# Kernel optimization log

Hardware: AMD Instinct MI355X
Metric: run time of the kernel (lower is better)

Reference implementation:

```python
import jax, jax.numpy as jnp
import numpy as np

N_NODES = 20000
N_EDGES = 640000
N_FEATS = 3703
HIDDEN = 50
N_CLASSES = 6
N_KENN_LAYERS = 3
# clause: not C_c(x) OR C_c(y) OR not Cite(x,y)  -> literal signs
SIGNS = np.array([-1.0, 1.0, -1.0], dtype=np.float32)


def setup_inputs() -> dict:
    key = jax.random.key(0)
    ks = jax.random.split(key, 12)
    features = jax.random.normal(ks[0], (N_NODES, N_FEATS), dtype=jnp.float32)
    relations = jax.random.normal(ks[1], (N_EDGES, 1), dtype=jnp.float32)
    sx = jax.random.randint(ks[2], (N_EDGES,), 0, N_NODES)
    sy = jax.random.randint(ks[3], (N_EDGES,), 0, N_NODES)

    def dense(k, fan_in, fan_out):
        return jax.random.normal(k, (fan_in, fan_out), dtype=jnp.float32) / np.sqrt(fan_in).astype(np.float32)

    W1 = dense(ks[4], N_FEATS, HIDDEN); b1 = jnp.zeros((HIDDEN,), jnp.float32)
    W2 = dense(ks[5], HIDDEN, HIDDEN);  b2 = jnp.zeros((HIDDEN,), jnp.float32)
    W3 = dense(ks[6], HIDDEN, HIDDEN);  b3 = jnp.zeros((HIDDEN,), jnp.float32)
    W4 = dense(ks[7], HIDDEN, N_CLASSES); b4 = jnp.zeros((N_CLASSES,), jnp.float32)
    # one learnable clause weight per class-clause, per KENN layer (init 0.5 as in KENN)
    clause_weights = jnp.full((N_KENN_LAYERS, N_CLASSES), 0.5, dtype=jnp.float32)
    return dict(features=features, relations=relations, sx=sx, sy=sy,
                W1=W1, b1=b1, W2=W2, b2=b2, W3=W3, b3=b3, W4=W4, b4=b4,
                clause_weights=clause_weights)


def _kenn_layer(z, relations, sx, sy, cw):
    # z: [N, C]; relations: [E, 1]; cw: [C] clause weights
    n = z.shape[0]
    zx = z[sx]                                   # [E, C] gather head literals
    zy = z[sy]                                   # [E, C] gather tail literals
    rel = jnp.broadcast_to(relations, (relations.shape[0], z.shape[1]))  # [E, C]
    signs = jnp.asarray(SIGNS)
    # signed literal preactivations per clause: [E, C, 3]
    v = jnp.stack([-zx, zy, -rel], axis=-1)
    # KENN boost: delta = w_c * softmax(signed preacts) * sign
    d = cw[None, :, None] * jax.nn.softmax(v, axis=-1) * signs[None, None, :]
    # scatter unary deltas back to nodes (relation delta is discarded)
    dz = jax.ops.segment_sum(d[..., 0], sx, num_segments=n)
    dz = dz + jax.ops.segment_sum(d[..., 1], sy, num_segments=n)
    return z + dz


def reference(features, relations, sx, sy, W1, b1, W2, b2, W3, b3, W4, b4, clause_weights):
    # MLP preactivations (dropout inactive at inference)
    x = jax.nn.relu(features @ W1 + b1)
    x = jax.nn.relu(x @ W2 + b2)
    x = jax.nn.relu(x @ W3 + b3)
    z = x @ W4 + b4                               # [N, 6]
    for i in range(N_KENN_LAYERS):
        z = _kenn_layer(z, relations, sx, sy, clause_weights[i])
    return jax.nn.softmax(z, axis=-1)
```

## Files before the change

kernel.cpp:

```cpp
#include <hip/hip_runtime.h>

#define M_NODES 20000
#define K_FEATS 3703
#define PADK 3712
#define NH 50
#define NC 6
#define N_EDGES_C 640000
#define NKB 116

typedef __attribute__((ext_vector_type(8))) __bf16 bf16x8;
typedef __attribute__((ext_vector_type(4))) float f32x4;

__global__ void k_packB(const float* __restrict__ W1, unsigned short* __restrict__ Bh,
                        unsigned short* __restrict__ Bl) {
  int idx = blockIdx.x * 256 + threadIdx.x;
  if (idx >= NKB * 4 * 64 * 8) return;
  int j = idx & 7;
  int lane = (idx >> 3) & 63;
  int t = (idx >> 9) & 3;
  int kb = idx >> 11;
  int k = kb * 32 + (lane >> 4) * 8 + j;
  int c = t * 16 + (lane & 15);
  float v = (k < K_FEATS && c < NH) ? W1[k * NH + c] : 0.f;
  __bf16 hb = (__bf16)v;
  float hf = (float)hb;
  __bf16 lb = (__bf16)(v - hf);
  Bh[idx] = *(unsigned short*)&hb;
  Bl[idx] = *(unsigned short*)&lb;
}

__global__ __launch_bounds__(256) void k_gemm1(const float* __restrict__ A,
    const unsigned short* __restrict__ Bph, const unsigned short* __restrict__ Bpl,
    float* __restrict__ part, int KS) {
  const int lane = threadIdx.x & 63;
  const int w = threadIdx.x >> 6;
  const int row0 = blockIdx.x * 128 + w * 32;
  const int s = blockIdx.y;
  const int ks = s * KS;
  const int ke = (ks + KS < PADK) ? ks + KS : PADK;
  const int nsteps = (ke - ks) >> 5;
  const int g = lane >> 4;
  const int rl = lane & 15;
  const int r0c = min(row0 + rl, M_NODES - 1);
  const int r1c = min(row0 + 16 + rl, M_NODES - 1);
  const float* a0p = A + (size_t)r0c * K_FEATS + 8 * g;
  const float* a1p = A + (size_t)r1c * K_FEATS + 8 * g;
  const bf16x8* BH = (const bf16x8*)Bph;
  const bf16x8* BL = (const bf16x8*)Bpl;

  f32x4 acc[2][4];
  #pragma unroll
  for (int i = 0; i < 2; ++i)
    #pragma unroll
    for (int t = 0; t < 4; ++t) acc[i][t] = (f32x4){0.f, 0.f, 0.f, 0.f};

  #define LOADA(d0, d1, k0) {                                     \
    d0[0] = *(const float4*)(a0p + (k0));                         \
    d0[1] = *(const float4*)(a0p + (k0) + 4);                     \
    d1[0] = *(const float4*)(a1p + (k0));                         \
    d1[1] = *(const float4*)(a1p + (k0) + 4); }
  #define LOADAG(d0, d1, k0) {                                    \
    _Pragma("unroll") for (int j = 0; j < 8; ++j) {               \
      int gk = (k0) + 8 * g + j;                                  \
      float v0 = (gk < K_FEATS) ? a0p[(k0) + j] : 0.f;            \
      float v1 = (gk < K_FEATS) ? a1p[(k0) + j] : 0.f;            \
      ((float*)d0)[j] = v0; ((float*)d1)[j] = v1; } }
  #define LDSEL(d0, d1, k0) {                                     \
    if ((k0) + 32 > K_FEATS) { LOADAG(d0, d1, k0) }               \
    else { LOADA(d0, d1, k0) } }

  #define BODY(sa0, sa1, k0) {                                    \
    const int kb4 = ((k0) >> 5) * 4;                              \
    bf16x8 bh0 = BH[(kb4 + 0) * 64 + lane];                       \
    bf16x8 bh1 = BH[(kb4 + 1) * 64 + lane];                       \
    bf16x8 bh2 = BH[(kb4 + 2) * 64 + lane];                       \
    bf16x8 bh3 = BH[(kb4 + 3) * 64 + lane];                       \
    bf16x8 bl0 = BL[(kb4 + 0) * 64 + lane];                       \
    bf16x8 bl1 = BL[(kb4 + 1) * 64 + lane];                       \
    bf16x8 bl2 = BL[(kb4 + 2) * 64 + lane];                       \
    bf16x8 bl3 = BL[(kb4 + 3) * 64 + lane];                       \
    bf16x8 ah0, al0, ah1, al1;                                    \
    _Pragma("unroll") for (int j = 0; j < 8; ++j) {               \
      float xv = ((const float*)sa0)[j];                          \
      __bf16 hb = (__bf16)xv; float hf = (float)hb;               \
      ah0[j] = hb; al0[j] = (__bf16)(xv - hf);                    \
      float yv = ((const float*)sa1)[j];                          \
      __bf16 hb2 = (__bf16)yv; float hf2 = (float)hb2;            \
      ah1[j] = hb2; al1[j] = (__bf16)(yv - hf2);                  \
    }                                                             \
    acc[0][0] = __builtin_amdgcn_mfma_f32_16x16x32_bf16(ah0, bh0, acc[0][0], 0, 0, 0); \
    acc[0][1] = __builtin_amdgcn_mfma_f32_16x16x32_bf16(ah0, bh1, acc[0][1], 0, 0, 0); \
    acc[0][2] = __builtin_amdgcn_mfma_f32_16x16x32_bf16(ah0, bh2, acc[0][2], 0, 0, 0); \
    acc[0][3] = __builtin_amdgcn_mfma_f32_16x16x32_bf16(ah0, bh3, acc[0][3], 0, 0, 0); \
    acc[1][0] = __builtin_amdgcn_mfma_f32_16x16x32_bf16(ah1, bh0, acc[1][0], 0, 0, 0); \
    acc[1][1] = __builtin_amdgcn_mfma_f32_16x16x32_bf16(ah1, bh1, acc[1][1], 0, 0, 0); \
    acc[1][2] = __builtin_amdgcn_mfma_f32_16x16x32_bf16(ah1, bh2, acc[1][2], 0, 0, 0); \
    acc[1][3] = __builtin_amdgcn_mfma_f32_16x16x32_bf16(ah1, bh3, acc[1][3], 0, 0, 0); \
    acc[0][0] = __builtin_amdgcn_mfma_f32_16x16x32_bf16(al0, bh0, acc[0][0], 0, 0, 0); \
    acc[0][1] = __builtin_amdgcn_mfma_f32_16x16x32_bf16(al0, bh1, acc[0][1], 0, 0, 0); \
    acc[0][2] = __builtin_amdgcn_mfma_f32_16x16x32_bf16(al0, bh2, acc[0][2], 0, 0, 0); \
    acc[0][3] = __builtin_amdgcn_mfma_f32_16x16x32_bf16(al0, bh3, acc[0][3], 0, 0, 0); \
    acc[1][0] = __builtin_amdgcn_mfma_f32_16x16x32_bf16(al1, bh0, acc[1][0], 0, 0, 0); \
    acc[1][1] = __builtin_amdgcn_mfma_f32_16x16x32_bf16(al1, bh1, acc[1][1], 0, 0, 0); \
    acc[1][2] = __builtin_amdgcn_mfma_f32_16x16x32_bf16(al1, bh2, acc[1][2], 0, 0, 0); \
    acc[1][3] = __builtin_amdgcn_mfma_f32_16x16x32_bf16(al1, bh3, acc[1][3], 0, 0, 0); \
    acc[0][0] = __builtin_amdgcn_mfma_f32_16x16x32_bf16(ah0, bl0, acc[0][0], 0, 0, 0); \
    acc[0][1] = __builtin_amdgcn_mfma_f32_16x16x32_bf16(ah0, bl1, acc[0][1], 0, 0, 0); \
    acc[0][2] = __builtin_amdgcn_mfma_f32_16x16x32_bf16(ah0, bl2, acc[0][2], 0, 0, 0); \
    acc[0][3] = __builtin_amdgcn_mfma_f32_16x16x32_bf16(ah0, bl3, acc[0][3], 0, 0, 0); \
    acc[1][0] = __builtin_amdgcn_mfma_f32_16x16x32_bf16(ah1, bl0, acc[1][0], 0, 0, 0); \
    acc[1][1] = __builtin_amdgcn_mfma_f32_16x16x32_bf16(ah1, bl1, acc[1][1], 0, 0, 0); \
    acc[1][2] = __builtin_amdgcn_mfma_f32_16x16x32_bf16(ah1, bl2, acc[1][2], 0, 0, 0); \
    acc[1][3] = __builtin_amdgcn_mfma_f32_16x16x32_bf16(ah1, bl3, acc[1][3], 0, 0, 0); }

  float4 p0a[2], p0b[2], p1a[2], p1b[2], p2a[2], p2b[2];
  LDSEL(p0a, p0b, ks);
  if (nsteps > 1) LDSEL(p1a, p1b, ks + 32);
  if (nsteps > 2) LDSEL(p2a, p2b, ks + 64);

  int t = 0;
  for (; t + 3 <= nsteps; t += 3) {
    const int k0 = ks + (t << 5);
    BODY(p0a, p0b, k0);
    if (t + 3 < nsteps) LDSEL(p0a, p0b, k0 + 96);
    BODY(p1a, p1b, k0 + 32);
    if (t + 4 < nsteps) LDSEL(p1a, p1b, k0 + 128);
    BODY(p2a, p2b, k0 + 64);
    if (t + 5 < nsteps) LDSEL(p2a, p2b, k0 + 160);
  }
  if (t < nsteps)     BODY(p0a, p0b, ks + (t << 5));
  if (t + 1 < nsteps) BODY(p1a, p1b, ks + ((t + 1) << 5));
  #undef LOADA
  #undef LOADAG
  #undef LDSEL
  #undef BODY

  float* p = part + (size_t)s * 1000000;
  #pragma unroll
  for (int i = 0; i < 2; ++i) {
    #pragma unroll
    for (int t2 = 0; t2 < 4; ++t2) {
      int col = t2 * 16 + rl;
      if (col < NH) {
        int rowb = row0 + i * 16 + g * 4;
        f32x4 v = acc[i][t2];
        #pragma unroll
        for (int q = 0; q < 4; ++q) {
          int row = rowb + q;
          if (row < M_NODES) p[row * NH + col] = v[q];
        }
      }
    }
  }
}

__global__ void k_epi(const float* __restrict__ part, const float* __restrict__ b1,
                      float* __restrict__ x1, int S) {
  int i = blockIdx.x * 256 + threadIdx.x;
  if (i >= M_NODES * NH) return;
  float v = b1[i % NH];
  for (int s = 0; s < S; ++s) v += part[(size_t)s * 1000000 + i];
  x1[i] = fmaxf(v, 0.f);
}

__global__ __launch_bounds__(256) void k_mlp(const float* __restrict__ x1,
    const float* __restrict__ W2, const float* __restrict__ b2,
    const float* __restrict__ W3, const float* __restrict__ b3,
    const float* __restrict__ W4, const float* __restrict__ b4,
    float* __restrict__ z) {
  __shared__ float lX[32 * 51];
  __shared__ float lW2[50 * 52];
  __shared__ float lW3[50 * 52];
  __shared__ float lW4[50 * 8];
  const int tid = threadIdx.x;
  const int row0 = blockIdx.x * 32;
  for (int idx = tid; idx < 2500; idx += 256) {
    int k = idx / 50, n = idx % 50;
    lW2[k * 52 + n] = W2[idx];
    lW3[k * 52 + n] = W3[idx];
  }
  for (int idx = tid; idx < 300; idx += 256) {
    int k = idx / 6, n = idx % 6;
    lW4[k * 8 + n] = W4[idx];
  }
  for (int idx = tid; idx < 1600; idx += 256) {
    int r = idx / 50, k = idx % 50;
    int gr = row0 + r;
    lX[r * 51 + k] = (gr < M_NODES) ? x1[gr * 50 + k] : 0.f;
  }
  __syncthreads();
  const int r = tid >> 3, cg = tid & 7;
  float x[50];
  #pragma unroll
  for (int k = 0; k < 50; ++k) x[k] = lX[r * 51 + k];

  for (int layer = 0; layer < 2; ++layer) {
    const float* lW = (layer == 0) ? lW2 : lW3;
    const float* bg = (layer == 0) ? b2 : b3;
    float acc[7];
    #pragma unroll
    for (int j = 0; j < 7; ++j) {
      int n = cg + 8 * j;
      acc[j] = (n < 50) ? bg[n] : 0.f;
    }
    #pragma unroll
    for (int k = 0; k < 50; ++k) {
      float xk = x[k];
      #pragma unroll
      for (int j = 0; j < 7; ++j) {
        int n = cg + 8 * j;
        if (n < 50) acc[j] = fmaf(xk, lW[k * 52 + n], acc[j]);
      }
    }
    __syncthreads();
    #pragma unroll
    for (int j = 0; j < 7; ++j) {
      int n = cg + 8 * j;
      if (n < 50) lX[r * 51 + n] = fmaxf(acc[j], 0.f);
    }
    __syncthreads();
    #pragma unroll
    for (int k = 0; k < 50; ++k) x[k] = lX[r * 51 + k];
  }
  if (cg < 6) {
    float accz = b4[cg];
    #pragma unroll
    for (int k = 0; k < 50; ++k) accz = fmaf(x[k], lW4[k * 8 + cg], accz);
    int gr = row0 + r;
    if (gr < M_NODES) z[gr * 6 + cg] = accz;
  }
}

__global__ void k_count(const int* __restrict__ sx, const int* __restrict__ sy,
                        int* __restrict__ cnt) {
  int e = blockIdx.x * 256 + threadIdx.x;
  if (e >= N_EDGES_C) return;
  atomicAdd(&cnt[sx[e]], 1);
  atomicAdd(&cnt[sy[e]], 1);
}

__global__ __launch_bounds__(1024) void k_scan(const int* __restrict__ cnt,
                                               int* __restrict__ off,
                                               int* __restrict__ cur) {
  __shared__ int sums[1024];
  int t = threadIdx.x;
  int base = t * 20;
  int local[20];
  int s = 0;
  #pragma unroll
  for (int j = 0; j < 20; ++j) {
    int idx = base + j;
    int v = (idx < M_NODES) ? cnt[idx] : 0;
    local[j] = s;
    s += v;
  }
  sums[t] = s;
  __syncthreads();
  for (int d = 1; d < 1024; d <<= 1) {
    int v = (t >= d) ? sums[t - d] : 0;
    __syncthreads();
    sums[t] += v;
    __syncthreads();
  }
  int excl = sums[t] - s;
  #pragma unroll
  for (int j = 0; j < 20; ++j) {
    int idx = base + j;
    if (idx < M_NODES) {
      int o = excl + local[j];
      off[idx] = o;
      cur[idx] = o;
    }
  }
  if (t == 1023) off[M_NODES] = sums[1023];
}

__global__ void k_scatter(const int* __restrict__ sx, const int* __restrict__ sy,
                          const float* __restrict__ rel,
                          int* __restrict__ cur, int2* __restrict__ ent) {
  int e = blockIdx.x * 256 + threadIdx.x;
  if (e >= N_EDGES_C) return;
  int a = sx[e], b = sy[e];
  int rb = __float_as_int(rel[e]);
  int p = atomicAdd(&cur[a], 1);
  ent[p] = make_int2((b << 1), rb);
  int q = atomicAdd(&cur[b], 1);
  ent[q] = make_int2((a << 1) | 1, rb);
}

__global__ __launch_bounds__(256) void k_gather(const float* __restrict__ z,
    const int* __restrict__ off, const int2* __restrict__ ent,
    const float* __restrict__ cw, float* __restrict__ partial) {
  int t = blockIdx.x * 256 + threadIdx.x;
  if (t >= M_NODES * 8) return;
  int s = t & 7;
  int n = t >> 3;
  int o0 = off[n];
  int deg = off[n + 1] - o0;
  int lo = o0 + ((deg * s) >> 3);
  int hi = o0 + ((deg * (s + 1)) >> 3);

  const float2* zr = (const float2*)(z + n * 6);
  float2 a0 = zr[0], a1 = zr[1], a2 = zr[2];
  float znv[6] = {a0.x, a0.y, a1.x, a1.y, a2.x, a2.y};
  float w[6];
  #pragma unroll
  for (int c = 0; c < 6; ++c) w[c] = cw[c];
  float dz[6] = {0.f, 0.f, 0.f, 0.f, 0.f, 0.f};

  for (int i = lo; i < hi; ++i) {
    int2 e2 = ent[i];
    int partner = e2.x >> 1;
    int side = e2.x & 1;
    float r = __int_as_float(e2.y);
    const float2* zp2 = (const float2*)(z + partner * 6);
    float2 p0 = zp2[0], p1 = zp2[1], p2 = zp2[2];
    float zpv[6] = {p0.x, p0.y, p1.x, p1.y, p2.x, p2.y};
    float v2 = -r;
    #pragma unroll
    for (int c = 0; c < 6; ++c) {
      float zx = side ? zpv[c] : znv[c];
      float zy = side ? znv[c] : zpv[c];
      float v0 = -zx, v1 = zy;
      float m = fmaxf(fmaxf(v0, v1), v2);
      float e0 = __expf(v0 - m);
      float e1 = __expf(v1 - m);
      float e2v = __expf(v2 - m);
      float inv = w[c] / (e0 + e1 + e2v);
      dz[c] += (side ? e1 : -e0) * inv;
    }
  }
  float* pp = partial + (size_t)s * 120000 + n * 6;
  #pragma unroll
  for (int c = 0; c < 6; ++c) pp[c] = dz[c];
}

__global__ void k_combine(const float* __restrict__ zc, const float* __restrict__ partial,
                          float* __restrict__ zn) {
  int i = blockIdx.x * 256 + threadIdx.x;
  if (i >= M_NODES * NC) return;
  float v = zc[i];
  #pragma unroll
  for (int s = 0; s < 8; ++s) v += partial[(size_t)s * 120000 + i];
  zn[i] = v;
}

__global__ void k_combine_softmax(const float* __restrict__ zc,
                                  const float* __restrict__ partial,
                                  float* __restrict__ out) {
  int n = blockIdx.x * 256 + threadIdx.x;
  if (n >= M_NODES) return;
  float v[6];
  #pragma unroll
  for (int c = 0; c < 6; ++c) v[c] = zc[n * 6 + c];
  #pragma unroll
  for (int s = 0; s < 8; ++s) {
    const float* pp = partial + (size_t)s * 120000 + n * 6;
    #pragma unroll
    for (int c = 0; c < 6; ++c) v[c] += pp[c];
  }
  float m = v[0];
  #pragma unroll
  for (int c = 1; c < 6; ++c) m = fmaxf(m, v[c]);
  float sum = 0.f, ev[6];
  #pragma unroll
  for (int c = 0; c < 6; ++c) { ev[c] = __expf(v[c] - m); sum += ev[c]; }
  float inv = 1.f / sum;
  float2* o2 = (float2*)(out + n * 6);
  o2[0] = make_float2(ev[0] * inv, ev[1] * inv);
  o2[1] = make_float2(ev[2] * inv, ev[3] * inv);
  o2[2] = make_float2(ev[4] * inv, ev[5] * inv);
}

extern "C" void kernel_launch(void* const* d_in, const int* in_sizes, int n_in,
                              void* d_out, int out_size, void* d_ws, size_t ws_size,
                              hipStream_t stream) {
  const float* A   = (const float*)d_in[0];
  const float* rel = (const float*)d_in[1];
  const int*   sx  = (const int*)d_in[2];
  const int*   sy  = (const int*)d_in[3];
  const float* W1  = (const float*)d_in[4];
  const float* b1  = (const float*)d_in[5];
  const float* W2  = (const float*)d_in[6];
  const float* b2  = (const float*)d_in[7];
  const float* W3  = (const float*)d_in[8];
  const float* b3  = (const float*)d_in[9];
  const float* W4  = (const float*)d_in[10];
  const float* b4  = (const float*)d_in[11];
  const float* cw  = (const float*)d_in[12];

  const int S = 8, KS = 512;

  float* base = (float*)d_ws;
  float* part = base;
  float* x1   = base + 8000000;
  float* zA   = base + 9000000;
  float* zB   = base + 9120000;
  unsigned short* Bph = (unsigned short*)(base + 9240000);
  unsigned short* Bpl = (unsigned short*)(base + 9360000);

  int*  cnt  = (int*)base;
  int*  off  = (int*)base + 24576;
  int*  cur  = (int*)base + 49152;
  int2* ent  = (int2*)((int*)base + 73728);
  float* partial = base + 2700000;

  k_packB<<<(NKB * 4 * 64 * 8 + 255) / 256, 256, 0, stream>>>(W1, Bph, Bpl);
  k_gemm1<<<dim3(157, S), 256, 0, stream>>>(A, Bph, Bpl, part, KS);
  k_epi<<<(M_NODES * NH + 255) / 256, 256, 0, stream>>>(part, b1, x1, S);
  k_mlp<<<(M_NODES + 31) / 32, 256, 0, stream>>>(x1, W2, b2, W3, b3, W4, b4, zA);

  hipMemsetAsync(cnt, 0, (M_NODES + 1) * sizeof(int), stream);
  k_count<<<(N_EDGES_C + 255) / 256, 256, 0, stream>>>(sx, sy, cnt);
  k_scan<<<1, 1024, 0, stream>>>(cnt, off, cur);
  k_scatter<<<(N_EDGES_C + 255) / 256, 256, 0, stream>>>(sx, sy, rel, cur, ent);

  float* zc = zA;
  float* zn = zB;
  for (int l = 0; l < 3; ++l) {
    k_gather<<<(M_NODES * 8 + 255) / 256, 256, 0, stream>>>(zc, off, ent, cw + 6 * l, partial);
    if (l < 2) {
      k_combine<<<(M_NODES * NC + 255) / 256, 256, 0, stream>>>(zc, partial, zn);
      float* t = zc; zc = zn; zn = t;
    } else {
      k_combine_softmax<<<(M_NODES + 255) / 256, 256, 0, stream>>>(zc, partial, (float*)d_out);
    }
  }
}
```

Before: 356.9 us.

## Fuse graph build and KENN layers into one cooperative persistent kernel

Replaces nine separate launches (count, scan, scatter, and the three gather/combine pairs) with a single cooperative kernel that uses grid-wide syncs between phases. The goal is to remove per-launch overhead and the tail gaps between the small graph kernels. In exchange, the grid is capped at 625 blocks, so large phases like the gather loop become grid-stride. The scan also now runs on a single 256-thread block with serial per-thread chunks, and each grid.sync adds its own barrier cost.

```diff
diff --git a/kernel.cpp b/kernel.cpp
--- a/kernel.cpp
+++ b/kernel.cpp
@@ -1,4 +1,7 @@
 #include <hip/hip_runtime.h>
+#include <hip/hip_cooperative_groups.h>
+
+namespace cg = cooperative_groups;
 
 #define M_NODES 20000
 #define K_FEATS 3703
@@ -7,6 +10,7 @@
 #define NC 6
 #define N_EDGES_C 640000
 #define NKB 116
+#define COOP_BLOCKS 625
 
 typedef __attribute__((ext_vector_type(8))) __bf16 bf16x8;
 typedef __attribute__((ext_vector_type(4))) float f32x4;
@@ -189,7 +193,7 @@
     lX[r * 51 + k] = (gr < M_NODES) ? x1[gr * 50 + k] : 0.f;
   }
   __syncthreads();
-  const int r = tid >> 3, cg = tid & 7;
+  const int r = tid >> 3, cg2 = tid & 7;
   float x[50];
   #pragma unroll
   for (int k = 0; k < 50; ++k) x[k] = lX[r * 51 + k];
@@ -200,7 +204,7 @@
     float acc[7];
     #pragma unroll
     for (int j = 0; j < 7; ++j) {
-      int n = cg + 8 * j;
+      int n = cg2 + 8 * j;
       acc[j] = (n < 50) ? bg[n] : 0.f;
     }
     #pragma unroll
@@ -208,168 +212,167 @@
       float xk = x[k];
       #pragma unroll
       for (int j = 0; j < 7; ++j) {
-        int n = cg + 8 * j;
+        int n = cg2 + 8 * j;
         if (n < 50) acc[j] = fmaf(xk, lW[k * 52 + n], acc[j]);
       }
     }
     __syncthreads();
     #pragma unroll
     for (int j = 0; j < 7; ++j) {
-      int n = cg + 8 * j;
+      int n = cg2 + 8 * j;
       if (n < 50) lX[r * 51 + n] = fmaxf(acc[j], 0.f);
     }
     __syncthreads();
     #pragma unroll
     for (int k = 0; k < 50; ++k) x[k] = lX[r * 51 + k];
   }
-  if (cg < 6) {
-    float accz = b4[cg];
-    #pragma unroll
-    for (int k = 0; k < 50; ++k) accz = fmaf(x[k], lW4[k * 8 + cg], accz);
+  if (cg2 < 6) {
+    float accz = b4[cg2];
+    #pragma unroll
+    for (int k = 0; k < 50; ++k) accz = fmaf(x[k], lW4[k * 8 + cg2], accz);
     int gr = row0 + r;
-    if (gr < M_NODES) z[gr * 6 + cg] = accz;
-  }
-}
-
-__global__ void k_count(const int* __restrict__ sx, const int* __restrict__ sy,
-                        int* __restrict__ cnt) {
-  int e = blockIdx.x * 256 + threadIdx.x;
-  if (e >= N_EDGES_C) return;
-  atomicAdd(&cnt[sx[e]], 1);
-  atomicAdd(&cnt[sy[e]], 1);
-}
-
-__global__ __launch_bounds__(1024) void k_scan(const int* __restrict__ cnt,
-                                               int* __restrict__ off,
-                                               int* __restrict__ cur) {
-  __shared__ int sums[1024];
-  int t = threadIdx.x;
-  int base = t * 20;
-  int local[20];
-  int s = 0;
-  #pragma unroll
-  for (int j = 0; j < 20; ++j) {
-    int idx = base + j;
-    int v = (idx < M_NODES) ? cnt[idx] : 0;
-    local[j] = s;
-    s += v;
-  }
-  sums[t] = s;
-  __syncthreads();
-  for (int d = 1; d < 1024; d <<= 1) {
-    int v = (t >= d) ? sums[t - d] : 0;
+    if (gr < M_NODES) z[gr * 6 + cg2] = accz;
+  }
+}
+
+__global__ __launch_bounds__(256) void k_kenn(
+    const int* __restrict__ sx, const int* __restrict__ sy,
+    const float* __restrict__ rel, int* __restrict__ cnt,
+    int* __restrict__ off, int* __restrict__ cur, int2* __restrict__ ent,
+    const float* __restrict__ cw, float* __restrict__ partial,
+    float* __restrict__ zA, float* __restrict__ zB, float* __restrict__ out) {
+  cg::grid_group grid = cg::this_grid();
+  const int tid0 = blockIdx.x * 256 + threadIdx.x;
+  const int stride = gridDim.x * 256;
+  __shared__ int sums[256];
+
+  for (int e = tid0; e < N_EDGES_C; e += stride) {
+    atomicAdd(&cnt[sx[e]], 1);
+    atomicAdd(&cnt[sy[e]], 1);
+  }
+  __threadfence();
+  grid.sync();
+
+  if (blockIdx.x == 0) {
+    int t = threadIdx.x;
+    int lo = t * 79;
+    int hi = lo + 79; if (hi > M_NODES) hi = M_NODES;
+    int s = 0;
+    for (int i = lo; i < hi; ++i) s += cnt[i];
+    sums[t] = s;
     __syncthreads();
-    sums[t] += v;
-    __syncthreads();
-  }
-  int excl = sums[t] - s;
-  #pragma unroll
-  for (int j = 0; j < 20; ++j) {
-    int idx = base + j;
-    if (idx < M_NODES) {
-      int o = excl + local[j];
-      off[idx] = o;
-      cur[idx] = o;
-    }
-  }
-  if (t == 1023) off[M_NODES] = sums[1023];
-}
-
-__global__ void k_scatter(const int* __restrict__ sx, const int* __restrict__ sy,
-                          const float* __restrict__ rel,
-                          int* __restrict__ cur, int2* __restrict__ ent) {
-  int e = blockIdx.x * 256 + threadIdx.x;
-  if (e >= N_EDGES_C) return;
-  int a = sx[e], b = sy[e];
-  int rb = __float_as_int(rel[e]);
-  int p = atomicAdd(&cur[a], 1);
-  ent[p] = make_int2((b << 1), rb);
-  int q = atomicAdd(&cur[b], 1);
-  ent[q] = make_int2((a << 1) | 1, rb);
-}
-
-__global__ __launch_bounds__(256) void k_gather(const float* __restrict__ z,
-    const int* __restrict__ off, const int2* __restrict__ ent,
-    const float* __restrict__ cw, float* __restrict__ partial) {
-  int t = blockIdx.x * 256 + threadIdx.x;
-  if (t >= M_NODES * 8) return;
-  int s = t & 7;
-  int n = t >> 3;
-  int o0 = off[n];
-  int deg = off[n + 1] - o0;
-  int lo = o0 + ((deg * s) >> 3);
-  int hi = o0 + ((deg * (s + 1)) >> 3);
-
-  const float2* zr = (const float2*)(z + n * 6);
-  float2 a0 = zr[0], a1 = zr[1], a2 = zr[2];
-  float znv[6] = {a0.x, a0.y, a1.x, a1.y, a2.x, a2.y};
-  float w[6];
-  #pragma unroll
-  for (int c = 0; c < 6; ++c) w[c] = cw[c];
-  float dz[6] = {0.f, 0.f, 0.f, 0.f, 0.f, 0.f};
-
-  for (int i = lo; i < hi; ++i) {
-    int2 e2 = ent[i];
-    int partner = e2.x >> 1;
-    int side = e2.x & 1;
-    float r = __int_as_float(e2.y);
-    const float2* zp2 = (const float2*)(z + partner * 6);
-    float2 p0 = zp2[0], p1 = zp2[1], p2 = zp2[2];
-    float zpv[6] = {p0.x, p0.y, p1.x, p1.y, p2.x, p2.y};
-    float v2 = -r;
-    #pragma unroll
-    for (int c = 0; c < 6; ++c) {
-      float zx = side ? zpv[c] : znv[c];
-      float zy = side ? znv[c] : zpv[c];
-      float v0 = -zx, v1 = zy;
-      float m = fmaxf(fmaxf(v0, v1), v2);
-      float e0 = __expf(v0 - m);
-      float e1 = __expf(v1 - m);
-      float e2v = __expf(v2 - m);
-      float inv = w[c] / (e0 + e1 + e2v);
-      dz[c] += (side ? e1 : -e0) * inv;
-    }
-  }
-  float* pp = partial + (size_t)s * 120000 + n * 6;
-  #pragma unroll
-  for (int c = 0; c < 6; ++c) pp[c] = dz[c];
-}
-
-__global__ void k_combine(const float* __restrict__ zc, const float* __restrict__ partial,
-                          float* __restrict__ zn) {
-  int i = blockIdx.x * 256 + threadIdx.x;
-  if (i >= M_NODES * NC) return;
-  float v = zc[i];
-  #pragma unroll
-  for (int s = 0; s < 8; ++s) v += partial[(size_t)s * 120000 + i];
-  zn[i] = v;
-}
-
-__global__ void k_combine_softmax(const float* __restrict__ zc,
-                                  const float* __restrict__ partial,
-                                  float* __restrict__ out) {
-  int n = blockIdx.x * 256 + threadIdx.x;
-  if (n >= M_NODES) return;
-  float v[6];
-  #pragma unroll
-  for (int c = 0; c < 6; ++c) v[c] = zc[n * 6 + c];
-  #pragma unroll
-  for (int s = 0; s < 8; ++s) {
-    const float* pp = partial + (size_t)s * 120000 + n * 6;
-    #pragma unroll
-    for (int c = 0; c < 6; ++c) v[c] += pp[c];
-  }
-  float m = v[0];
-  #pragma unroll
-  for (int c = 1; c < 6; ++c) m = fmaxf(m, v[c]);
-  float sum = 0.f, ev[6];
-  #pragma unroll
-  for (int c = 0; c < 6; ++c) { ev[c] = __expf(v[c] - m); sum += ev[c]; }
-  float inv = 1.f / sum;
-  float2* o2 = (float2*)(out + n * 6);
-  o2[0] = make_float2(ev[0] * inv, ev[1] * inv);
-  o2[1] = make_float2(ev[2] * inv, ev[3] * inv);
-  o2[2] = make_float2(ev[4] * inv, ev[5] * inv);
+    for (int d = 1; d < 256; d <<= 1) {
+      int v = (t >= d) ? sums[t - d] : 0;
+      __syncthreads();
+      sums[t] += v;
+      __syncthreads();
+    }
+    int run = sums[t] - s;
+    for (int i = lo; i < hi; ++i) {
+      off[i] = run;
+      cur[i] = run;
+      run += cnt[i];
+    }
+    if (t == 255) off[M_NODES] = sums[255];
+  }
+  __threadfence();
+  grid.sync();
+
+  for (int e = tid0; e < N_EDGES_C; e += stride) {
+    int a = sx[e], b = sy[e];
+    int rb = __float_as_int(rel[e]);
+    int p = atomicAdd(&cur[a], 1);
+    ent[p] = make_int2((b << 1), rb);
+    int q = atomicAdd(&cur[b], 1);
+    ent[q] = make_int2((a << 1) | 1, rb);
+  }
+  __threadfence();
+  grid.sync();
+
+  for (int l = 0; l < 3; ++l) {
+    const float* zc = (l & 1) ? zB : zA;
+    float* zn = (l & 1) ? zA : zB;
+    const float* w6 = cw + 6 * l;
+
+    for (int t = tid0; t < M_NODES * 8; t += stride) {
+      int s = t & 7;
+      int n = t >> 3;
+      int o0 = off[n];
+      int deg = off[n + 1] - o0;
+      int lo = o0 + ((deg * s) >> 3);
+      int hi = o0 + ((deg * (s + 1)) >> 3);
+
+      const float2* zr = (const float2*)(zc + n * 6);
+      float2 a0 = zr[0], a1 = zr[1], a2 = zr[2];
+      float znv[6] = {a0.x, a0.y, a1.x, a1.y, a2.x, a2.y};
+      float w[6];
+      #pragma unroll
+      for (int c = 0; c < 6; ++c) w[c] = w6[c];
+      float dz[6] = {0.f, 0.f, 0.f, 0.f, 0.f, 0.f};
+
+      for (int i = lo; i < hi; ++i) {
+        int2 e2 = ent[i];
+        int partner = e2.x >> 1;
+        int side = e2.x & 1;
+        float r = __int_as_float(e2.y);
+        const float2* zp2 = (const float2*)(zc + partner * 6);
+        float2 p0 = zp2[0], p1 = zp2[1], p2 = zp2[2];
+        float zpv[6] = {p0.x, p0.y, p1.x, p1.y, p2.x, p2.y};
+        float v2 = -r;
+        #pragma unroll
+        for (int c = 0; c < 6; ++c) {
+          float zx = side ? zpv[c] : znv[c];
+          float zy = side ? znv[c] : zpv[c];
+          float v0 = -zx, v1 = zy;
+          float m = fmaxf(fmaxf(v0, v1), v2);
+          float e0 = __expf(v0 - m);
+          float e1 = __expf(v1 - m);
+          float e2v = __expf(v2 - m);
+          float inv = w[c] / (e0 + e1 + e2v);
+          dz[c] += (side ? e1 : -e0) * inv;
+        }
+      }
+      float* pp = partial + (size_t)s * 120000 + n * 6;
+      #pragma unroll
+      for (int c = 0; c < 6; ++c) pp[c] = dz[c];
+    }
+    __threadfence();
+    grid.sync();
+
+    if (l < 2) {
+      for (int i = tid0; i < M_NODES * NC; i += stride) {
+        float v = zc[i];
+        #pragma unroll
+        for (int s = 0; s < 8; ++s) v += partial[(size_t)s * 120000 + i];
+        zn[i] = v;
+      }
+      __threadfence();
+      grid.sync();
+    } else {
+      for (int n = tid0; n < M_NODES; n += stride) {
+        float v[6];
+        #pragma unroll
+        for (int c = 0; c < 6; ++c) v[c] = zc[n * 6 + c];
+        #pragma unroll
+        for (int s = 0; s < 8; ++s) {
+          const float* pp = partial + (size_t)s * 120000 + n * 6;
+          #pragma unroll
+          for (int c = 0; c < 6; ++c) v[c] += pp[c];
+        }
+        float m = v[0];
+        #pragma unroll
+        for (int c = 1; c < 6; ++c) m = fmaxf(m, v[c]);
+        float sum = 0.f, ev[6];
+        #pragma unroll
+        for (int c = 0; c < 6; ++c) { ev[c] = __expf(v[c] - m); sum += ev[c]; }
+        float inv = 1.f / sum;
+        float2* o2 = (float2*)(out + n * 6);
+        o2[0] = make_float2(ev[0] * inv, ev[1] * inv);
+        o2[1] = make_float2(ev[2] * inv, ev[3] * inv);
+        o2[2] = make_float2(ev[4] * inv, ev[5] * inv);
+      }
+    }
+  }
 }
 
 extern "C" void kernel_launch(void* const* d_in, const int* in_sizes, int n_in,
@@ -404,6 +407,7 @@
   int*  cur  = (int*)base + 49152;
   int2* ent  = (int2*)((int*)base + 73728);
   float* partial = base + 2700000;
+  float* outp = (float*)d_out;
 
   k_packB<<<(NKB * 4 * 64 * 8 + 255) / 256, 256, 0, stream>>>(W1, Bph, Bpl);
   k_gemm1<<<dim3(157, S), 256, 0, stream>>>(A, Bph, Bpl, part, KS);
@@ -411,19 +415,11 @@
   k_mlp<<<(M_NODES + 31) / 32, 256, 0, stream>>>(x1, W2, b2, W3, b3, W4, b4, zA);
 
   hipMemsetAsync(cnt, 0, (M_NODES + 1) * sizeof(int), stream);
-  k_count<<<(N_EDGES_C + 255) / 256, 256, 0, stream>>>(sx, sy, cnt);
-  k_scan<<<1, 1024, 0, stream>>>(cnt, off, cur);
-  k_scatter<<<(N_EDGES_C + 255) / 256, 256, 0, stream>>>(sx, sy, rel, cur, ent);
-
-  float* zc = zA;
-  float* zn = zB;
-  for (int l = 0; l < 3; ++l) {
-    k_gather<<<(M_NODES * 8 + 255) / 256, 256, 0, stream>>>(zc, off, ent, cw + 6 * l, partial);
-    if (l < 2) {
-      k_combine<<<(M_NODES * NC + 255) / 256, 256, 0, stream>>>(zc, partial, zn);
-      float* t = zc; zc = zn; zn = t;
-    } else {
-      k_combine_softmax<<<(M_NODES + 255) / 256, 256, 0, stream>>>(zc, partial, (float*)d_out);
-    }
-  }
-}
+
+  void* args[] = {
+    (void*)&sx, (void*)&sy, (void*)&rel, (void*)&cnt, (void*)&off, (void*)&cur,
+    (void*)&ent, (void*)&cw, (void*)&partial, (void*)&zA, (void*)&zB, (void*)&outp
+  };
+  hipLaunchCooperativeKernel((void*)k_kenn, dim3(COOP_BLOCKS), dim3(256),
+                             args, 0, stream);
+}
```

Result: slower. 1.410 ms (+295.0%).
